# Performance work log

Hardware: AMD Instinct MI355X
Metric: run time of the kernel (lower is better)

The kernel has to match this reference:

```python
import jax, jax.numpy as jnp
import numpy as np

B, C, N = 4, 128, 8192
CQK = C // 4  # query/key projection dim = out_channels // 4


def setup_inputs() -> dict:
    key = jax.random.key(0)
    ks = jax.random.split(key, 9)
    s_in = 1.0 / np.sqrt(C)
    return {
        "x": jax.random.normal(ks[0], (B, C, N), dtype=jnp.float32),
        "xyz": jax.random.normal(ks[1], (B, N, 3), dtype=jnp.float32),
        "Wq": jax.random.normal(ks[2], (CQK, C), dtype=jnp.float32) * s_in,
        "bq": jax.random.normal(ks[3], (CQK,), dtype=jnp.float32) * 0.01,
        "Wk": jax.random.normal(ks[4], (CQK, C), dtype=jnp.float32) * s_in,
        "bk": jax.random.normal(ks[5], (CQK,), dtype=jnp.float32) * 0.01,
        "Wv": jax.random.normal(ks[6], (C, C), dtype=jnp.float32) * s_in,
        "bv": jax.random.normal(ks[7], (C,), dtype=jnp.float32) * 0.01,
        "gamma": jax.random.normal(ks[8], (1,), dtype=jnp.float32) * 0.1,
    }


def reference(x, xyz, Wq, bq, Wk, bk, Wv, bv, gamma):
    # 1x1 Conv1d == per-point linear projection over channels
    q = jnp.einsum('oc,bcn->bon', Wq, x) + bq[None, :, None]   # (B, CQK, N)
    k = jnp.einsum('oc,bcn->bon', Wk, x) + bk[None, :, None]   # (B, CQK, N)
    v = jnp.einsum('oc,bcn->bon', Wv, x) + bv[None, :, None]   # (B, C, N)

    # energy[b, n, m] = <q[:, n], k[:, m]>
    energy = jnp.einsum('bcn,bcm->bnm', q, k)                  # (B, N, N)

    # positional correlation bias: normalize coords per point, cosine-sim matrix
    xyz_bcn = jnp.swapaxes(xyz, 1, 2)                          # (B, 3, N)
    xyz_norm = xyz_bcn / (jnp.linalg.norm(xyz_bcn, axis=1, keepdims=True) + 1e-8)
    pos_corr = jnp.einsum('bcn,bcm->bnm', xyz_norm, xyz_norm)  # (B, N, N)
    energy = energy + 0.1 * pos_corr

    attention = jax.nn.softmax(energy, axis=-1)                # rowwise over m

    # out[b, c, n] = sum_m v[b, c, m] * attention[b, n, m]
    out = jnp.einsum('bcm,bnm->bcn', v, attention)             # (B, C, N)
    return gamma * out + x
```

## Files before the change

### kernel.cpp

```cpp
#include <hip/hip_runtime.h>

#define NPTS 8192
#define NB 4
#define NCH 128
#define DQK 48
#define TK 64
#define SPLIT 4
#define KEYS_PER (NPTS / SPLIT)
#define ROUNDS (KEYS_PER / TK)
#define SH2 28.853901f
#define LOG2E 1.4426950408889634f

typedef unsigned short ushort_t;
typedef unsigned int uint_t;
typedef __attribute__((ext_vector_type(8))) short bf16x8;
typedef __attribute__((ext_vector_type(2))) float f32x2;
typedef __attribute__((ext_vector_type(4))) float f32x4;
typedef __attribute__((ext_vector_type(16))) float f32x16;

static __device__ __forceinline__ ushort_t f2bf(float x) {
  union { float f; uint_t u; } v; v.f = x;
  uint_t r = v.u + 0x7fffu + ((v.u >> 16) & 1u);
  return (ushort_t)(r >> 16);
}
static __device__ __forceinline__ float bf2f(ushort_t u) {
  union { uint_t i; float f; } v; v.i = ((uint_t)u) << 16; return v.f;
}
static __device__ __forceinline__ int sig16(int n) {
  int g2 = (n >> 2) & 3;
  return (g2 == 1 || g2 == 2) ? (n ^ 0xC) : n;
}

typedef __attribute__((address_space(1))) void void_g;
typedef __attribute__((address_space(3))) void void_l;
static __device__ __forceinline__ void gload_lds16(const ushort_t* g, ushort_t* l) {
  __builtin_amdgcn_global_load_lds((void_g*)(ushort_t*)g, (void_l*)l, 16, 0, 0);
}


#define TPITCH 40
#define WBELEMS (6 * 8 * 64 * 8)
__global__ __launch_bounds__(512, 2)
void projm2_kernel(const float* __restrict__ x, const float* __restrict__ xyz,
                   const float* __restrict__ Wq, const float* __restrict__ bq,
                   const float* __restrict__ Wk, const float* __restrict__ bk,
                   const float* __restrict__ Wv, const float* __restrict__ bv,
                   ushort_t* __restrict__ Qb, ushort_t* __restrict__ Kb,
                   ushort_t* __restrict__ Vt) {
  __shared__ __align__(16) ushort_t WbL[WBELEMS];
  __shared__ float biasL[192];
  __shared__ __align__(16) ushort_t T[8][32 * TPITCH];
  const int tid = threadIdx.x;
  const int lane = tid & 63, wv = tid >> 6;
  const int l31 = lane & 31, h = lane >> 5;
  const int b = blockIdx.y;
  const int tile = wv >> 1, half = wv & 1;
  const int n0 = blockIdx.x * 128 + tile * 32;
  const int n = n0 + l31;

  bf16x8 bfr[8];
  const float* xb = x + (size_t)b * NCH * NPTS + n;
#pragma unroll
  for (int ks = 0; ks < 8; ++ks) {
    const float* xc = xb + (size_t)(ks * 16 + h * 8) * NPTS;
    union { ushort_t u[8]; bf16x8 v; } p;
#pragma unroll
    for (int j = 0; j < 8; ++j) p.u[j] = f2bf(xc[(size_t)j * NPTS]);
    bfr[ks] = p.v;
  }

#pragma unroll
  for (int it = 0; it < 6; ++it) {
    int slot = tid + it * 512;
    int zk = slot >> 6, ln = slot & 63;
    int z = zk >> 3, ks = zk & 7;
    const float* W = (z == 0) ? Wq : (z == 1) ? Wk
                                              : (Wv + (size_t)(z - 2) * 32 * 128);
    const float sc = (z == 0) ? LOG2E : 1.0f;
    const float* wr = W + (ln & 31) * 128 + ks * 16 + (ln >> 5) * 8;
    union { ushort_t u[8]; bf16x8 v; } p;
#pragma unroll
    for (int j = 0; j < 8; ++j) p.u[j] = f2bf(wr[j] * sc);
    *(bf16x8*)(WbL + (size_t)slot * 8) = p.v;
  }
  if (tid < 192)
    biasL[tid] = (tid < 32) ? bq[tid] * LOG2E
                            : (tid < 64) ? bk[tid - 32] : bv[tid - 64];

  float xa = xyz[((size_t)b * NPTS + n) * 3 + 0];
  float xc2 = xyz[((size_t)b * NPTS + n) * 3 + 1];
  float xd = xyz[((size_t)b * NPTS + n) * 3 + 2];
  float rinv = 1.0f / (sqrtf(xa * xa + xc2 * xc2 + xd * xd) + 1e-8f);

  __syncthreads();

  const int nploc = (l31 & 16) | sig16(l31 & 15);
  ushort_t* tw = &T[wv][0];

#pragma unroll 1
  for (int zz = 0; zz < 3; ++zz) {
    const int z = half * 3 + zz;
    f32x16 S;
#pragma unroll
    for (int r = 0; r < 16; ++r)
      S[r] = biasL[z * 32 + (r & 3) + 8 * (r >> 2) + 4 * h];
#pragma unroll
    for (int ks = 0; ks < 8; ++ks) {
      bf16x8 af = *(const bf16x8*)(WbL + ((size_t)(z * 8 + ks) * 64 + lane) * 8);
      S = __builtin_amdgcn_mfma_f32_32x32x16_bf16(af, bfr[ks], S, 0, 0, 0);
    }
    if (z <= 1) {
#pragma unroll
      for (int r = 0; r < 16; ++r)
        tw[l31 * TPITCH + (r & 3) + 8 * (r >> 2) + 4 * h] = f2bf(S[r]);
      ushort_t* dstf = (z == 0 ? Qb : Kb) +
                       (((size_t)b * 256 + (n0 >> 5)) * 3) * 512;
#pragma unroll
      for (int c = 0; c < 2; ++c) {
        bf16x8 fr = *(const bf16x8*)&tw[(lane & 31) * TPITCH + c * 16 + (lane >> 5) * 8];
        *(bf16x8*)(dstf + c * 512 + lane * 8) = fr;
      }
      float sc = (z == 0) ? LOG2E : 1.0f;
      float rn = 0.31622776601683794f * sc * rinv;
      union { ushort_t u[16]; bf16x8 v[2]; } t;
#pragma unroll
      for (int j = 0; j < 16; ++j) t.u[j] = 0;
      t.u[0] = f2bf(xa * rn); t.u[1] = f2bf(xc2 * rn); t.u[2] = f2bf(xd * rn);
      t.u[3] = (z == 0) ? f2bf(-SH2) : f2bf(1.0f);
      *(bf16x8*)(dstf + 1024 + l31 * 8) = t.v[0];
      *(bf16x8*)(dstf + 1024 + 256 + l31 * 8) = t.v[1];
    } else {
#pragma unroll
      for (int r = 0; r < 16; ++r)
        tw[((r & 3) + 8 * (r >> 2) + 4 * h) * TPITCH + nploc] = f2bf(S[r]);
#pragma unroll
      for (int g = 0; g < 2; ++g) {
        bf16x8 fr = *(const bf16x8*)&tw[(lane & 31) * TPITCH + g * 16 + (lane >> 5) * 8];
        int kk = ((n0 >> 4) + g) & 3;
        ushort_t* dst = Vt + ((((size_t)b * 128 + (n0 >> 6)) * 16 +
                               (z - 2) * 4 + kk) * 512);
        *(bf16x8*)(dst + lane * 8) = fr;
      }
    }
  }
}

__global__ __launch_bounds__(512, 4)
void attn32_kernel(const ushort_t* __restrict__ Qb, const ushort_t* __restrict__ Kb,
                   const ushort_t* __restrict__ Vt,
                   ushort_t* __restrict__ PACC, float* __restrict__ PL) {
  __shared__ __align__(16) ushort_t L[2][22][512];
  const int tid = threadIdx.x;
  const int lane = tid & 63, w = tid >> 6;

  const int lin = blockIdx.x;
  const int bs = lin & 15;
  const int b = bs & 3, sseg = bs >> 2;
  const int qblk = lin >> 4;
  const int q0w = qblk * 256 + w * 32;
  const int m00 = sseg * KEYS_PER;

  bf16x8 qf[3];
  {
    const ushort_t* qbase = Qb + (((size_t)b * 256 + (q0w >> 5)) * 3) * 512 + lane * 8;
#pragma unroll
    for (int c = 0; c < 3; ++c) qf[c] = *(const bf16x8*)(qbase + c * 512);
  }

  const ushort_t* vbase = Vt + (((size_t)b * 128 + (m00 >> 6)) * 16) * 512 + lane * 8;
  const ushort_t* kbase = Kb + (((size_t)b * 256 + (m00 >> 5)) * 3) * 512 + lane * 8;
  const ushort_t* gp[3];
  int fid[3], adv[3];
  const int nf = (w < 6) ? 3 : 2;
#pragma unroll
  for (int i = 0; i < 3; ++i) {
    int fi = w + 8 * i;
    fid[i] = fi;
    if (fi < 16) { gp[i] = vbase + fi * 512; adv[i] = 16 * 512; }
    else if (fi < 22) { gp[i] = kbase + (fi - 16) * 512; adv[i] = 6 * 512; }
  }

  f32x16 O[4];
#pragma unroll
  for (int f = 0; f < 4; ++f) O[f] = (f32x16)(0.f);
  float ls0 = 0.f, ls1 = 0.f;

#pragma unroll
  for (int i = 0; i < 3; ++i)
    if (i < nf) gload_lds16(gp[i], &L[0][fid[i]][0]);

#pragma unroll 1
  for (int t = 0; t < ROUNDS; ++t) {
    __syncthreads();
    const int cur = t & 1;
    if (t + 1 < ROUNDS) {
#pragma unroll
      for (int i = 0; i < 3; ++i)
        if (i < nf) {
          gp[i] += adv[i];
          gload_lds16(gp[i], &L[cur ^ 1][fid[i]][0]);
        }
    }

#pragma unroll
    for (int kb = 0; kb < 2; ++kb) {
      bf16x8 kf0 = *(const bf16x8*)(&L[cur][16 + kb * 3 + 0][0] + lane * 8);
      bf16x8 kf1 = *(const bf16x8*)(&L[cur][16 + kb * 3 + 1][0] + lane * 8);
      bf16x8 kf2 = *(const bf16x8*)(&L[cur][16 + kb * 3 + 2][0] + lane * 8);

      __builtin_amdgcn_s_setprio(1);
      f32x16 S = __builtin_amdgcn_mfma_f32_32x32x16_bf16(kf0, qf[0],
                                                         (f32x16)(0.f), 0, 0, 0);
      S = __builtin_amdgcn_mfma_f32_32x32x16_bf16(kf1, qf[1], S, 0, 0, 0);
      S = __builtin_amdgcn_mfma_f32_32x32x16_bf16(kf2, qf[2], S, 0, 0, 0);
      __builtin_amdgcn_s_setprio(0);

      uint_t pk[8];
#pragma unroll
      for (int i = 0; i < 8; ++i) {
        float p0 = __builtin_amdgcn_exp2f(S[2 * i]);
        float p1 = __builtin_amdgcn_exp2f(S[2 * i + 1]);
        ls0 += p0;
        ls1 += p1;
        pk[i] = __builtin_amdgcn_perm(__float_as_uint(p1), __float_as_uint(p0),
                                      0x07060302u);
      }

#pragma unroll
      for (int kkl = 0; kkl < 2; ++kkl) {
        union { uint_t u[4]; bf16x8 v; } au;
        au.u[0] = pk[4 * kkl + 0];
        au.u[1] = pk[4 * kkl + 1];
        au.u[2] = pk[4 * kkl + 2];
        au.u[3] = pk[4 * kkl + 3];
        bf16x8 A = au.v;
        __builtin_amdgcn_s_setprio(1);
#pragma unroll
        for (int f = 0; f < 4; ++f) {
          bf16x8 vf = *(const bf16x8*)(&L[cur][f * 4 + kb * 2 + kkl][0] + lane * 8);
          O[f] = __builtin_amdgcn_mfma_f32_32x32x16_bf16(A, vf, O[f], 0, 0, 0);
        }
        __builtin_amdgcn_s_setprio(0);
      }
    }
  }

  float lsum = ls0 + ls1;
  lsum += __shfl_xor(lsum, 32);
  const size_t pbase = (size_t)(bs * 16 + (qblk >> 1)) * 16 + (qblk & 1) * 8 + w;
#pragma unroll
  for (int f = 0; f < 4; ++f) {
    union { ushort_t u[16]; bf16x8 v[2]; } pu;
#pragma unroll
    for (int r = 0; r < 16; ++r) pu.u[r] = f2bf(O[f][r]);
    size_t idx = (pbase * 4 + f) * 1024 + (size_t)lane * 16;
    *(bf16x8*)(PACC + idx) = pu.v[0];
    *(bf16x8*)(PACC + idx + 8) = pu.v[1];
  }
  if (lane < 32) PL[(size_t)bs * NPTS + q0w + lane] = lsum;
}

#define MP2 132
__global__ __launch_bounds__(256, 4)
void merge4c_kernel(const ushort_t* __restrict__ PACC, const float* __restrict__ PL,
                    const float* __restrict__ x, const float* __restrict__ gamma,
                    float* __restrict__ out) {
  __shared__ float Linv[128];
  __shared__ float ldso[32 * MP2];
  const int tid = threadIdx.x;
  const int qb = blockIdx.x, b = blockIdx.y, f = blockIdx.z;
  const int q0 = qb * 128;

  if (tid < 128) {
    float Ls = 0.f;
#pragma unroll
    for (int s = 0; s < 4; ++s)
      Ls += PL[(size_t)(s * 4 + b) * NPTS + q0 + tid];
    Linv[tid] = gamma[0] / Ls;
  }
  __syncthreads();

  const int ww = tid >> 6, lane = tid & 63, l31 = lane & 31, h = lane >> 5;

  float acc[16];
#pragma unroll
  for (int r = 0; r < 16; ++r) acc[r] = 0.f;
#pragma unroll
  for (int s = 0; s < 4; ++s) {
    size_t idx = (((size_t)(s * 4 + b) * 256 + (q0 >> 5) + ww) * 4 + f) * 1024 +
                 (size_t)lane * 16;
    bf16x8 a0 = *(const bf16x8*)(PACC + idx);
    bf16x8 a1 = *(const bf16x8*)(PACC + idx + 8);
#pragma unroll
    for (int r = 0; r < 8; ++r) {
      acc[r] += bf2f((ushort_t)a0[r]);
      acc[8 + r] += bf2f((ushort_t)a1[r]);
    }
  }
  const int qloc = ww * 32 + 4 * h;
#pragma unroll
  for (int rr = 0; rr < 4; ++rr) {
    int q = qloc + 8 * rr;
    f32x4 v;
#pragma unroll
    for (int i = 0; i < 4; ++i) v[i] = acc[rr * 4 + i] * Linv[q + i];
    *(f32x4*)&ldso[l31 * MP2 + q] = v;
  }
  __syncthreads();

  const float* xb = x + ((size_t)b * NCH + f * 32) * NPTS + q0;
  float* ob = out + ((size_t)b * NCH + f * 32) * NPTS + q0;
#pragma unroll
  for (int rr = 0; rr < 8; ++rr) {
    int ch = ww * 8 + rr;
    f32x2 v = *(const f32x2*)&ldso[ch * MP2 + lane * 2];
    f32x2 xv = *(const f32x2*)(xb + (size_t)ch * NPTS + lane * 2);
    v += xv;
    *(f32x2*)(ob + (size_t)ch * NPTS + lane * 2) = v;
  }
}

extern "C" void kernel_launch(void* const* d_in, const int* in_sizes, int n_in,
                              void* d_out, int out_size, void* d_ws,
                              size_t ws_size, hipStream_t stream) {
  const float* x     = (const float*)d_in[0];
  const float* xyz   = (const float*)d_in[1];
  const float* Wq    = (const float*)d_in[2];
  const float* bq    = (const float*)d_in[3];
  const float* Wk    = (const float*)d_in[4];
  const float* bk    = (const float*)d_in[5];
  const float* Wv    = (const float*)d_in[6];
  const float* bv    = (const float*)d_in[7];
  const float* gamma = (const float*)d_in[8];
  float* out = (float*)d_out;

  const size_t BN = (size_t)NB * NPTS;
  ushort_t* Qb = (ushort_t*)d_ws;
  ushort_t* Kb = Qb + BN * DQK;
  ushort_t* Vt = Kb + BN * DQK;
  ushort_t* PACC = Vt + BN * NCH;
  float* PL = (float*)(PACC + (size_t)16 * 16 * 8 * 2 * 4 * 1024);

  projm2_kernel<<<dim3(NPTS / 128, NB), 512, 0, stream>>>(
      x, xyz, Wq, bq, Wk, bk, Wv, bv, Qb, Kb, Vt);
  attn32_kernel<<<512, 512, 0, stream>>>(Qb, Kb, Vt, PACC, PL);
  merge4c_kernel<<<dim3(64, NB, 4), 256, 0, stream>>>(PACC, PL, x, gamma, out);
  (void)in_sizes; (void)n_in; (void)out_size; (void)ws_size;
}
```

Before: 181.6 us.

## Fuse split-K merge into attention kernel via last-arriving-block atomic counter

Removes the separate merge kernel launch. Each attention block publishes its partial accumulators, fences, and increments a per-(batch, query-block) counter that the projection kernel resets. The fourth block to arrive sums the partials, normalizes by the combined softmax denominators, adds the residual, and writes the output. This saves one kernel launch and its scheduling gap, at the cost of a serialized tail merge done by a few blocks and reliance on memory fences for correctness.

```diff
diff --git a/kernel.cpp b/kernel.cpp
--- a/kernel.cpp
+++ b/kernel.cpp
@@ -46,7 +46,7 @@
                    const float* __restrict__ Wk, const float* __restrict__ bk,
                    const float* __restrict__ Wv, const float* __restrict__ bv,
                    ushort_t* __restrict__ Qb, ushort_t* __restrict__ Kb,
-                   ushort_t* __restrict__ Vt) {
+                   ushort_t* __restrict__ Vt, int* __restrict__ cnt) {
   __shared__ __align__(16) ushort_t WbL[WBELEMS];
   __shared__ float biasL[192];
   __shared__ __align__(16) ushort_t T[8][32 * TPITCH];
@@ -58,6 +58,8 @@
   const int n0 = blockIdx.x * 128 + tile * 32;
   const int n = n0 + l31;
 
+  if (blockIdx.x == 0 && blockIdx.y == 0 && tid < 128) cnt[tid] = 0;
+
   bf16x8 bfr[8];
   const float* xb = x + (size_t)b * NCH * NPTS + n;
 #pragma unroll
@@ -148,8 +150,11 @@
 __global__ __launch_bounds__(512, 4)
 void attn32_kernel(const ushort_t* __restrict__ Qb, const ushort_t* __restrict__ Kb,
                    const ushort_t* __restrict__ Vt,
-                   ushort_t* __restrict__ PACC, float* __restrict__ PL) {
+                   ushort_t* __restrict__ PACC, float* __restrict__ PL,
+                   int* __restrict__ cnt, const float* __restrict__ x,
+                   const float* __restrict__ gma, float* __restrict__ out) {
   __shared__ __align__(16) ushort_t L[2][22][512];
+  __shared__ int ordS;
   const int tid = threadIdx.x;
   const int lane = tid & 63, w = tid >> 6;
 
@@ -258,65 +263,58 @@
     *(bf16x8*)(PACC + idx + 8) = pu.v[1];
   }
   if (lane < 32) PL[(size_t)bs * NPTS + q0w + lane] = lsum;
-}
-
-#define MP2 132
-__global__ __launch_bounds__(256, 4)
-void merge4c_kernel(const ushort_t* __restrict__ PACC, const float* __restrict__ PL,
-                    const float* __restrict__ x, const float* __restrict__ gamma,
-                    float* __restrict__ out) {
-  __shared__ float Linv[128];
-  __shared__ float ldso[32 * MP2];
-  const int tid = threadIdx.x;
-  const int qb = blockIdx.x, b = blockIdx.y, f = blockIdx.z;
-  const int q0 = qb * 128;
-
-  if (tid < 128) {
+
+  __threadfence();
+  __syncthreads();
+  if (tid == 0) ordS = atomicAdd(&cnt[b * 32 + qblk], 1);
+  __syncthreads();
+  if (ordS != 3) return;
+  __threadfence();
+
+  float* Lf = (float*)&L[0][0][0];
+  float* LinvS = Lf;
+  float* bw = Lf + 256 + w * (32 * 33);
+  const int q0b = qblk * 256;
+  if (tid < 256) {
     float Ls = 0.f;
 #pragma unroll
     for (int s = 0; s < 4; ++s)
-      Ls += PL[(size_t)(s * 4 + b) * NPTS + q0 + tid];
-    Linv[tid] = gamma[0] / Ls;
+      Ls += PL[(size_t)(b + 4 * s) * NPTS + q0b + tid];
+    LinvS[tid] = gma[0] / Ls;
   }
   __syncthreads();
 
-  const int ww = tid >> 6, lane = tid & 63, l31 = lane & 31, h = lane >> 5;
-
-  float acc[16];
-#pragma unroll
-  for (int r = 0; r < 16; ++r) acc[r] = 0.f;
-#pragma unroll
-  for (int s = 0; s < 4; ++s) {
-    size_t idx = (((size_t)(s * 4 + b) * 256 + (q0 >> 5) + ww) * 4 + f) * 1024 +
-                 (size_t)lane * 16;
-    bf16x8 a0 = *(const bf16x8*)(PACC + idx);
-    bf16x8 a1 = *(const bf16x8*)(PACC + idx + 8);
-#pragma unroll
-    for (int r = 0; r < 8; ++r) {
-      acc[r] += bf2f((ushort_t)a0[r]);
-      acc[8 + r] += bf2f((ushort_t)a1[r]);
-    }
-  }
-  const int qloc = ww * 32 + 4 * h;
-#pragma unroll
-  for (int rr = 0; rr < 4; ++rr) {
-    int q = qloc + 8 * rr;
-    f32x4 v;
-#pragma unroll
-    for (int i = 0; i < 4; ++i) v[i] = acc[rr * 4 + i] * Linv[q + i];
-    *(f32x4*)&ldso[l31 * MP2 + q] = v;
-  }
-  __syncthreads();
-
-  const float* xb = x + ((size_t)b * NCH + f * 32) * NPTS + q0;
-  float* ob = out + ((size_t)b * NCH + f * 32) * NPTS + q0;
-#pragma unroll
-  for (int rr = 0; rr < 8; ++rr) {
-    int ch = ww * 8 + rr;
-    f32x2 v = *(const f32x2*)&ldso[ch * MP2 + lane * 2];
-    f32x2 xv = *(const f32x2*)(xb + (size_t)ch * NPTS + lane * 2);
-    v += xv;
-    *(f32x2*)(ob + (size_t)ch * NPTS + lane * 2) = v;
+  const int l31m = lane & 31, hm = lane >> 5;
+#pragma unroll 1
+  for (int f = 0; f < 4; ++f) {
+    float acc[16];
+#pragma unroll
+    for (int r = 0; r < 16; ++r) acc[r] = 0.f;
+#pragma unroll
+    for (int s = 0; s < 4; ++s) {
+      size_t pb = (size_t)((b + 4 * s) * 16 + (qblk >> 1)) * 16 + (qblk & 1) * 8 + w;
+      size_t idx = (pb * 4 + f) * 1024 + (size_t)lane * 16;
+      bf16x8 a0 = *(const bf16x8*)(PACC + idx);
+      bf16x8 a1 = *(const bf16x8*)(PACC + idx + 8);
+#pragma unroll
+      for (int r = 0; r < 8; ++r) {
+        acc[r] += bf2f((ushort_t)a0[r]);
+        acc[8 + r] += bf2f((ushort_t)a1[r]);
+      }
+    }
+#pragma unroll
+    for (int r = 0; r < 16; ++r) {
+      int qr = (r & 3) + 8 * (r >> 2) + 4 * hm;
+      bw[l31m * 33 + qr] = acc[r] * LinvS[w * 32 + qr];
+    }
+    const float* xf = x + ((size_t)b * NCH + f * 32) * NPTS + q0b + w * 32;
+    float* of = out + ((size_t)b * NCH + f * 32) * NPTS + q0b + w * 32;
+#pragma unroll
+    for (int it = 0; it < 16; ++it) {
+      int ch = it * 2 + hm;
+      float v = bw[ch * 33 + l31m] + xf[(size_t)ch * NPTS + l31m];
+      of[(size_t)ch * NPTS + l31m] = v;
+    }
   }
 }
 
@@ -340,10 +338,10 @@
   ushort_t* Vt = Kb + BN * DQK;
   ushort_t* PACC = Vt + BN * NCH;
   float* PL = (float*)(PACC + (size_t)16 * 16 * 8 * 2 * 4 * 1024);
+  int* cnt = (int*)(PL + (size_t)16 * NPTS);
 
   projm2_kernel<<<dim3(NPTS / 128, NB), 512, 0, stream>>>(
-      x, xyz, Wq, bq, Wk, bk, Wv, bv, Qb, Kb, Vt);
-  attn32_kernel<<<512, 512, 0, stream>>>(Qb, Kb, Vt, PACC, PL);
-  merge4c_kernel<<<dim3(64, NB, 4), 256, 0, stream>>>(PACC, PL, x, gamma, out);
+      x, xyz, Wq, bq, Wk, bk, Wv, bv, Qb, Kb, Vt, cnt);
+  attn32_kernel<<<512, 512, 0, stream>>>(Qb, Kb, Vt, PACC, PL, cnt, x, gamma, out);
   (void)in_sizes; (void)n_in; (void)out_size; (void)ws_size;
 }
```

Result: slower. 359.7 us (+98.1%).
